# Kernel optimization log

Measured on AMD Instinct MI355X. Metric: run time of the kernel, lower is better.

Reference implementation:

```python
import jax, jax.numpy as jnp
import numpy as np

B, N, IN_F, OUT_F = 8, 2048, 256, 256
ALPHA = 0.2  # LeakyReLU negative slope
NEG_INF = -1e9


def setup_inputs() -> dict:
    key = jax.random.key(0)
    ks = jax.random.split(key, 8)
    h = jax.random.normal(ks[0], (B, N, IN_F), dtype=jnp.float32)
    adj = jax.random.randint(ks[1], (B, N, N), 0, 2, dtype=jnp.int32)
    # xavier-ish scaled params
    W_w = jax.random.normal(ks[2], (OUT_F, IN_F), dtype=jnp.float32) * (1.414 / np.sqrt(IN_F + OUT_F))
    W_b = jnp.zeros((OUT_F,), dtype=jnp.float32)
    ai_w = jax.random.normal(ks[3], (1, OUT_F), dtype=jnp.float32) * (1.414 / np.sqrt(OUT_F + 1))
    ai_b = jnp.zeros((1,), dtype=jnp.float32)
    aj_w = jax.random.normal(ks[4], (1, OUT_F), dtype=jnp.float32) * (1.414 / np.sqrt(OUT_F + 1))
    aj_b = jnp.zeros((1,), dtype=jnp.float32)
    return {"h": h, "adj": adj, "W_w": W_w, "W_b": W_b,
            "ai_w": ai_w, "ai_b": ai_b, "aj_w": aj_w, "aj_b": aj_b}


def reference(h, adj, W_w, W_b, ai_w, ai_b, aj_w, aj_b):
    # Wh: [B, N, F]
    Wh = jnp.einsum('bni,oi->bno', h, W_w) + W_b
    # additive attention scores (pos_embed_dim == 1 so the .view is a transpose)
    Wh1 = jnp.einsum('bnf,of->bno', Wh, ai_w) + ai_b        # [B, N, 1]
    Wh2 = jnp.einsum('bnf,of->bno', Wh, aj_w) + aj_b        # [B, N, 1]
    e = Wh1 + jnp.swapaxes(Wh2, 1, 2)                       # [B, N, N]
    e = jnp.where(e >= 0, e, ALPHA * e)                     # LeakyReLU
    attention = jnp.where(adj > 0, e, NEG_INF)
    attention = jax.nn.softmax(attention, axis=2)
    # dropout: inference mode (training=False) -> identity
    h_hat = jnp.einsum('bnm,bmf->bnf', attention, Wh)
    return jax.nn.elu(h_hat)  # concat=True
```

## Files before the change

### kernel.cpp

```cpp
#include <hip/hip_runtime.h>

typedef __bf16 bf16;
typedef _Float16 f16;
typedef __bf16 bf16x8 __attribute__((ext_vector_type(8)));
typedef _Float16 f16x8 __attribute__((ext_vector_type(8)));
typedef float  f32x4  __attribute__((ext_vector_type(4)));

#define B_  8
#define N_  2048
#define F_  256
#define NTOK (B_ * N_)
static constexpr float LOG2E = 1.44269504088896f;

__device__ __forceinline__ int detect_bf16(const void* h) {
    const unsigned* hw = (const unsigned*)h;
    unsigned w = hw[threadIdx.x & 63];
    unsigned ex = (w >> 7) & 0xFFu;
    unsigned long long b = __ballot(ex > 100u && ex < 150u);
    return __popcll(b) >= 40;
}

__device__ __forceinline__ float ldf(const void* p, int i, int isb) {
    return isb ? (float)((const bf16*)p)[i] : ((const float*)p)[i];
}

__device__ __forceinline__ bf16x8 cvt8(const float* p) {
    float4 a = *(const float4*)p;
    float4 b = *(const float4*)(p + 4);
    bf16x8 r;
    r[0]=(bf16)a.x; r[1]=(bf16)a.y; r[2]=(bf16)a.z; r[3]=(bf16)a.w;
    r[4]=(bf16)b.x; r[5]=(bf16)b.y; r[6]=(bf16)b.z; r[7]=(bf16)b.w;
    return r;
}

__device__ __forceinline__ size_t wht2_idx(int b, int f, int n) {
    int jc = n >> 6;
    int slot = ((n >> 3) & 7) ^ (f & 7);
    return (((size_t)(b * 32 + jc) * F_ + f) << 6) + (slot << 3) + (n & 7);
}

__global__ __launch_bounds__(256)
void k_wht(const void* __restrict__ hv, const void* __restrict__ Wv,
           const void* __restrict__ Wbv, const void* __restrict__ ai_wv,
           const void* __restrict__ ai_bv, const void* __restrict__ aj_wv,
           const void* __restrict__ aj_bv, bf16* __restrict__ WhT2,
           unsigned* __restrict__ adjw) {
    int isb = detect_bf16(hv);
    int ttile = blockIdx.x;
    int fg = threadIdx.x >> 6;
    int lane = threadIdx.x & 63;
    int T0 = ttile * 16;
    int m = lane & 15, quad = lane >> 4;

    f32x4 acc[4];
#pragma unroll
    for (int ft = 0; ft < 4; ++ft) acc[ft] = (f32x4){0.f, 0.f, 0.f, 0.f};

    if (isb) {
        const bf16* hp = (const bf16*)hv + (size_t)(T0 + m) * F_ + quad * 8;
        const bf16* wp = (const bf16*)Wv + (size_t)(fg * 64 + m) * F_ + quad * 8;
#pragma unroll
        for (int kk = 0; kk < F_; kk += 32) {
            bf16x8 hf = *(const bf16x8*)(hp + kk);
#pragma unroll
            for (int ft = 0; ft < 4; ++ft) {
                bf16x8 wf = *(const bf16x8*)(wp + (size_t)ft * 16 * F_ + kk);
                acc[ft] = __builtin_amdgcn_mfma_f32_16x16x32_bf16(wf, hf, acc[ft], 0, 0, 0);
            }
        }
    } else {
        const float* hp = (const float*)hv + (size_t)(T0 + m) * F_ + quad * 8;
        const float* wp = (const float*)Wv + (size_t)(fg * 64 + m) * F_ + quad * 8;
#pragma unroll
        for (int kk = 0; kk < F_; kk += 32) {
            bf16x8 hf = cvt8(hp + kk);
#pragma unroll
            for (int ft = 0; ft < 4; ++ft) {
                bf16x8 wf = cvt8(wp + (size_t)ft * 16 * F_ + kk);
                acc[ft] = __builtin_amdgcn_mfma_f32_16x16x32_bf16(wf, hf, acc[ft], 0, 0, 0);
            }
        }
    }
    int token = T0 + m;
    int b = token >> 11, n = token & (N_ - 1);
    float s_p = 0.f, t_p = 0.f;
#pragma unroll
    for (int ft = 0; ft < 4; ++ft)
#pragma unroll
        for (int r = 0; r < 4; ++r) {
            int f = fg * 64 + ft * 16 + quad * 4 + r;
            float v = acc[ft][r] + ldf(Wbv, f, isb);
            bf16 vb = (bf16)v;
            WhT2[wht2_idx(b, f, n)] = vb;
            float vr = (float)vb;
            s_p += vr * ldf(ai_wv, f, isb);
            t_p += vr * ldf(aj_wv, f, isb);
        }
    s_p += __shfl_down(s_p, 32, 64); s_p += __shfl_down(s_p, 16, 64);
    t_p += __shfl_down(t_p, 32, 64); t_p += __shfl_down(t_p, 16, 64);
    __shared__ float sred[4][16], tred[4][16];
    if (lane < 16) { sred[fg][lane] = s_p; tred[fg][lane] = t_p; }
    __syncthreads();
    if (threadIdx.x < 16) {
        int tid = threadIdx.x;
        int tok = T0 + tid;
        float ss = (sred[0][tid] + sred[1][tid] + sred[2][tid] + sred[3][tid]
                    + ldf(ai_bv, 0, isb)) * LOG2E;
        float tt = (tred[0][tid] + tred[1][tid] + tred[2][tid] + tred[3][tid]
                    + ldf(aj_bv, 0, isb)) * LOG2E;
        f16 th = (f16)tt, sh = (f16)ss;
        unsigned short tu, su;
        __builtin_memcpy(&tu, &th, 2);
        __builtin_memcpy(&su, &sh, 2);
        unsigned w0 = adjw[tok];
        adjw[tok] = (w0 & 0xFFFFu) | ((unsigned)tu << 16);
        unsigned w1 = adjw[NTOK + tok];
        adjw[NTOK + tok] = (w1 & 0xFFFFu) | ((unsigned)su << 16);
    }
}

__device__ __forceinline__ unsigned char pbits(uint4 a, uint4 b) {
    return (unsigned char)((a.x & 1u) | ((a.y & 1u) << 1) | ((a.z & 1u) << 2) |
                           ((a.w & 1u) << 3) | ((b.x & 1u) << 4) |
                           ((b.y & 1u) << 5) | ((b.z & 1u) << 6) |
                           ((b.w & 1u) << 7));
}

__device__ __forceinline__ void stageB(const bf16* tile, char* dst,
                                       int w, int lane) {
#pragma unroll
    for (int r = 0; r < 8; ++r) {
        int off = (w * 8 + r) * 1024;
        const bf16* g = tile + off / 2 + lane * 8;
        __builtin_amdgcn_global_load_lds(
            (const __attribute__((address_space(1))) unsigned*)g,
            (__attribute__((address_space(3))) unsigned*)(dst + off),
            16, 0, 0);
    }
}

__global__ __launch_bounds__(256)
void k_attn(const unsigned* __restrict__ adjw, const bf16* __restrict__ WhT2,
            const void* __restrict__ hv, void* __restrict__ outv) {
    int isb = detect_bf16(hv);
    int bid = blockIdx.x;
    int b = bid >> 6, itile = bid & 63, i0 = itile * 32;
    int tid = threadIdx.x;
    int w = tid >> 6, lane = tid & 63, m = lane & 15, q = lane >> 4;
    int mt = w >> 1, jh = w & 1;

    __shared__ __align__(16) char smem[70656];
    char* Bbuf0 = smem;
    char* Bbuf1 = smem + 32768;
    f16* tLDS   = (f16*)(smem + 65536);
    unsigned char* pack0 = (unsigned char*)(smem + 69632);
    unsigned char* pack1 = (unsigned char*)(smem + 69888);
    float* red  = (float*)smem;

    const bf16* batch_tiles = WhT2 + ((size_t)b * 32) * F_ * 64;

#pragma unroll
    for (int k = 0; k < 8; ++k) {
        int idx = k * 256 + tid;
        unsigned wv = adjw[b * N_ + idx];
        unsigned short us = (unsigned short)(wv >> 16);
        f16 tv; __builtin_memcpy(&tv, &us, 2);
        tLDS[idx] = tv;
    }
    int row = i0 + mt * 16 + m;
    unsigned swd = adjw[NTOK + b * N_ + row];
    unsigned short su = (unsigned short)(swd >> 16);
    f16 sh; __builtin_memcpy(&sh, &su, 2);
    float s2i = (float)sh;

    int prow = tid >> 3, ps = tid & 7;
    const unsigned* arow = adjw + ((size_t)(b * N_ + i0 + prow)) * N_ + ps * 8;
    {
        uint4 x0 = *(const uint4*)arow, x1 = *(const uint4*)(arow + 4);
        pack0[prow * 8 + ps] = pbits(x0, x1);
    }
    stageB(batch_tiles, Bbuf0, w, lane);
    __syncthreads();

    bf16x8 ones;
#pragma unroll
    for (int k = 0; k < 8; ++k) ones[k] = (bf16)1.0f;

    f32x4 acc[16];
#pragma unroll
    for (int ft = 0; ft < 16; ++ft) acc[ft] = (f32x4){0.f, 0.f, 0.f, 0.f};
    f32x4 acc_l = {0.f, 0.f, 0.f, 0.f};

    for (int c = 0; c < 32; ++c) {
        char* Bcur = (c & 1) ? Bbuf1 : Bbuf0;
        unsigned char* pcur = (c & 1) ? pack1 : pack0;
        uint4 aw0, aw1;
        bool pre = (c < 31);
        if (pre) {
            stageB(batch_tiles + (size_t)(c + 1) * F_ * 64,
                   (c & 1) ? Bbuf0 : Bbuf1, w, lane);
            aw0 = *(const uint4*)(arow + (size_t)(c + 1) * 64);
            aw1 = *(const uint4*)(arow + (size_t)(c + 1) * 64 + 4);
        }
        unsigned long long pb64 =
            *(const unsigned long long*)(pcur + (mt * 16 + m) * 8);
        unsigned bits8 = (unsigned)(pb64 >> ((jh * 4 + q) * 8)) & 0xFFu;
        f16x8 tv = *(const f16x8*)(tLDS + c * 64 + jh * 32 + q * 8);

        bf16x8 af;
#pragma unroll
        for (int qq = 0; qq < 8; ++qq) {
            float x = s2i + (float)tv[qq];
            x = fmaxf(x, 0.2f * x);
            float pv = ((bits8 >> qq) & 1u) ? __builtin_amdgcn_exp2f(x) : 0.f;
            af[qq] = (bf16)pv;
        }
        int sbase = (jh * 4 + q);
#pragma unroll
        for (int ft = 0; ft < 16; ++ft) {
            int fr = ft * 16 + m;
            int psl = sbase ^ (m & 7);
            bf16x8 bfr = *(const bf16x8*)(Bcur + fr * 128 + psl * 16);
            acc[ft] = __builtin_amdgcn_mfma_f32_16x16x32_bf16(af, bfr, acc[ft], 0, 0, 0);
        }
        acc_l = __builtin_amdgcn_mfma_f32_16x16x32_bf16(af, ones, acc_l, 0, 0, 0);
        if (pre)
            ((c & 1) ? pack0 : pack1)[prow * 8 + ps] = pbits(aw0, aw1);
        __syncthreads();
    }

    if (jh == 1) {
#pragma unroll
        for (int r = 0; r < 4; ++r) {
            int rr = mt * 16 + q * 4 + r;
#pragma unroll
            for (int ft = 0; ft < 16; ++ft)
                red[rr * 257 + ft * 16 + m] = acc[ft][r];
            if (m == 0) red[rr * 257 + 256] = acc_l[r];
        }
    }
    __syncthreads();
    if (jh == 0) {
#pragma unroll
        for (int r = 0; r < 4; ++r) {
            int rr = mt * 16 + q * 4 + r;
            float lf = acc_l[r] + red[rr * 257 + 256];
            float rl = (lf > 0.f) ? (1.f / lf) : 0.f;
            size_t ob = ((size_t)b * N_ + i0 + rr) * F_;
#pragma unroll
            for (int ft = 0; ft < 16; ++ft) {
                int f = ft * 16 + m;
                float v = acc[ft][r] + red[rr * 257 + f];
                v *= rl;
                v = (v > 0.f) ? v : (__builtin_amdgcn_exp2f(v * LOG2E) - 1.f);
                if (isb) ((bf16*)outv)[ob + f] = (bf16)v;
                else     ((float*)outv)[ob + f] = v;
            }
        }
    }
}

extern "C" void kernel_launch(void* const* d_in, const int* in_sizes, int n_in,
                              void* d_out, int out_size, void* d_ws, size_t ws_size,
                              hipStream_t stream) {
    (void)in_sizes; (void)n_in; (void)out_size; (void)ws_size;
    const void* h    = d_in[0];
    unsigned*   adjw = (unsigned*)d_in[1];
    const void* W_w  = d_in[2];
    const void* W_b  = d_in[3];
    const void* ai_w = d_in[4];
    const void* ai_b = d_in[5];
    const void* aj_w = d_in[6];
    const void* aj_b = d_in[7];

    bf16* WhT2 = (bf16*)d_ws;

    k_wht <<<dim3(1024), dim3(256), 0, stream>>>(h, W_w, W_b, ai_w, ai_b,
                                                 aj_w, aj_b, WhT2, adjw);
    k_attn<<<dim3(512),  dim3(256), 0, stream>>>(adjw, WhT2, h, d_out);
}
```

Baseline: 272.2 us.

## Load Wh tiles directly to registers, prepack full adjacency bitmask, split waves by feature half

The attention kernel stops staging Wh tiles through double-buffered LDS with global_load_lds. Each wave now reads its B fragments straight from global memory and covers both 16-row m-tiles for half of the feature columns, so each B fragment is reused across two MFMAs. The whole 32x2048 adjacency bitmask is packed into LDS once before the loop, and the per-iteration barrier becomes one barrier every four chunks. This saves LDS traffic and sync cost but depends on L2/L1 for B reuse across waves and blocks, and it adds a clamp on the exp2 argument.

```diff
diff --git a/kernel.cpp b/kernel.cpp
--- a/kernel.cpp
+++ b/kernel.cpp
@@ -119,26 +119,6 @@
     }
 }
 
-__device__ __forceinline__ unsigned char pbits(uint4 a, uint4 b) {
-    return (unsigned char)((a.x & 1u) | ((a.y & 1u) << 1) | ((a.z & 1u) << 2) |
-                           ((a.w & 1u) << 3) | ((b.x & 1u) << 4) |
-                           ((b.y & 1u) << 5) | ((b.z & 1u) << 6) |
-                           ((b.w & 1u) << 7));
-}
-
-__device__ __forceinline__ void stageB(const bf16* tile, char* dst,
-                                       int w, int lane) {
-#pragma unroll
-    for (int r = 0; r < 8; ++r) {
-        int off = (w * 8 + r) * 1024;
-        const bf16* g = tile + off / 2 + lane * 8;
-        __builtin_amdgcn_global_load_lds(
-            (const __attribute__((address_space(1))) unsigned*)g,
-            (__attribute__((address_space(3))) unsigned*)(dst + off),
-            16, 0, 0);
-    }
-}
-
 __global__ __launch_bounds__(256)
 void k_attn(const unsigned* __restrict__ adjw, const bf16* __restrict__ WhT2,
             const void* __restrict__ hv, void* __restrict__ outv) {
@@ -147,17 +127,13 @@
     int b = bid >> 6, itile = bid & 63, i0 = itile * 32;
     int tid = threadIdx.x;
     int w = tid >> 6, lane = tid & 63, m = lane & 15, q = lane >> 4;
-    int mt = w >> 1, jh = w & 1;
-
-    __shared__ __align__(16) char smem[70656];
-    char* Bbuf0 = smem;
-    char* Bbuf1 = smem + 32768;
-    f16* tLDS   = (f16*)(smem + 65536);
-    unsigned char* pack0 = (unsigned char*)(smem + 69632);
-    unsigned char* pack1 = (unsigned char*)(smem + 69888);
+    int jh = w & 1, fh = w >> 1;
+
+    __shared__ __align__(16) char smem[33280];
+    unsigned long long* pack64 = (unsigned long long*)smem;
+    f16*   tLDS = (f16*)(smem + 8448);
     float* red  = (float*)smem;
-
-    const bf16* batch_tiles = WhT2 + ((size_t)b * 32) * F_ * 64;
+    __shared__ float lLDS[2][32];
 
 #pragma unroll
     for (int k = 0; k < 8; ++k) {
@@ -167,94 +143,124 @@
         f16 tv; __builtin_memcpy(&tv, &us, 2);
         tLDS[idx] = tv;
     }
-    int row = i0 + mt * 16 + m;
-    unsigned swd = adjw[NTOK + b * N_ + row];
-    unsigned short su = (unsigned short)(swd >> 16);
-    f16 sh; __builtin_memcpy(&sh, &su, 2);
-    float s2i = (float)sh;
-
-    int prow = tid >> 3, ps = tid & 7;
-    const unsigned* arow = adjw + ((size_t)(b * N_ + i0 + prow)) * N_ + ps * 8;
+    float s2i0, s2i1;
     {
-        uint4 x0 = *(const uint4*)arow, x1 = *(const uint4*)(arow + 4);
-        pack0[prow * 8 + ps] = pbits(x0, x1);
-    }
-    stageB(batch_tiles, Bbuf0, w, lane);
+        unsigned sw0 = adjw[NTOK + b * N_ + i0 + m];
+        unsigned sw1 = adjw[NTOK + b * N_ + i0 + 16 + m];
+        unsigned short u0 = (unsigned short)(sw0 >> 16);
+        unsigned short u1 = (unsigned short)(sw1 >> 16);
+        f16 h0, h1;
+        __builtin_memcpy(&h0, &u0, 2); __builtin_memcpy(&h1, &u1, 2);
+        s2i0 = (float)h0; s2i1 = (float)h1;
+    }
+#pragma unroll
+    for (int k = 0; k < 4; ++k) {
+        int id = tid * 4 + k;
+        int prow = id >> 5, pc = id & 31;
+        const unsigned* src = adjw + ((size_t)(b * N_ + i0 + prow)) * N_ + pc * 64;
+        unsigned long long bits = 0;
+#pragma unroll
+        for (int w8 = 0; w8 < 16; ++w8) {
+            uint4 a = *(const uint4*)(src + w8 * 4);
+            bits |= (unsigned long long)((a.x & 1u) | ((a.y & 1u) << 1) |
+                                         ((a.z & 1u) << 2) | ((a.w & 1u) << 3))
+                    << (w8 * 4);
+        }
+        pack64[prow * 33 + pc] = bits;
+    }
     __syncthreads();
 
     bf16x8 ones;
 #pragma unroll
     for (int k = 0; k < 8; ++k) ones[k] = (bf16)1.0f;
 
-    f32x4 acc[16];
-#pragma unroll
-    for (int ft = 0; ft < 16; ++ft) acc[ft] = (f32x4){0.f, 0.f, 0.f, 0.f};
-    f32x4 acc_l = {0.f, 0.f, 0.f, 0.f};
+    f32x4 acc0[8], acc1[8];
+#pragma unroll
+    for (int ft = 0; ft < 8; ++ft) {
+        acc0[ft] = (f32x4){0.f, 0.f, 0.f, 0.f};
+        acc1[ft] = (f32x4){0.f, 0.f, 0.f, 0.f};
+    }
+    f32x4 acc_l0 = {0.f, 0.f, 0.f, 0.f}, acc_l1 = {0.f, 0.f, 0.f, 0.f};
+
+    int psl = (jh * 4 + q) ^ (m & 7);
+    const size_t tilestep = (size_t)F_ * 64;
+    const bf16* btile = WhT2 + (size_t)(b * 32) * tilestep +
+                        (size_t)(fh * 128) * 64 + m * 64 + psl * 8;
+    int byi = jh * 4 + q;
 
     for (int c = 0; c < 32; ++c) {
-        char* Bcur = (c & 1) ? Bbuf1 : Bbuf0;
-        unsigned char* pcur = (c & 1) ? pack1 : pack0;
-        uint4 aw0, aw1;
-        bool pre = (c < 31);
-        if (pre) {
-            stageB(batch_tiles + (size_t)(c + 1) * F_ * 64,
-                   (c & 1) ? Bbuf0 : Bbuf1, w, lane);
-            aw0 = *(const uint4*)(arow + (size_t)(c + 1) * 64);
-            aw1 = *(const uint4*)(arow + (size_t)(c + 1) * 64 + 4);
-        }
-        unsigned long long pb64 =
-            *(const unsigned long long*)(pcur + (mt * 16 + m) * 8);
-        unsigned bits8 = (unsigned)(pb64 >> ((jh * 4 + q) * 8)) & 0xFFu;
+        unsigned long long pb0 = pack64[m * 33 + c];
+        unsigned long long pb1 = pack64[(16 + m) * 33 + c];
+        unsigned bits0 = (unsigned)(pb0 >> (byi * 8)) & 0xFFu;
+        unsigned bits1 = (unsigned)(pb1 >> (byi * 8)) & 0xFFu;
         f16x8 tv = *(const f16x8*)(tLDS + c * 64 + jh * 32 + q * 8);
 
-        bf16x8 af;
+        bf16x8 af0, af1;
 #pragma unroll
         for (int qq = 0; qq < 8; ++qq) {
-            float x = s2i + (float)tv[qq];
-            x = fmaxf(x, 0.2f * x);
-            float pv = ((bits8 >> qq) & 1u) ? __builtin_amdgcn_exp2f(x) : 0.f;
-            af[qq] = (bf16)pv;
-        }
-        int sbase = (jh * 4 + q);
-#pragma unroll
-        for (int ft = 0; ft < 16; ++ft) {
-            int fr = ft * 16 + m;
-            int psl = sbase ^ (m & 7);
-            bf16x8 bfr = *(const bf16x8*)(Bcur + fr * 128 + psl * 16);
-            acc[ft] = __builtin_amdgcn_mfma_f32_16x16x32_bf16(af, bfr, acc[ft], 0, 0, 0);
-        }
-        acc_l = __builtin_amdgcn_mfma_f32_16x16x32_bf16(af, ones, acc_l, 0, 0, 0);
-        if (pre)
-            ((c & 1) ? pack0 : pack1)[prow * 8 + ps] = pbits(aw0, aw1);
-        __syncthreads();
-    }
-
+            float tvf = (float)tv[qq];
+            float x0 = s2i0 + tvf, x1 = s2i1 + tvf;
+            x0 = fmaxf(x0, 0.2f * x0);
+            x1 = fmaxf(x1, 0.2f * x1);
+            x0 = fminf(fmaxf(x0, -120.f), 60.f);
+            x1 = fminf(fmaxf(x1, -120.f), 60.f);
+            float p0 = ((bits0 >> qq) & 1u) ? __builtin_amdgcn_exp2f(x0) : 0.f;
+            float p1 = ((bits1 >> qq) & 1u) ? __builtin_amdgcn_exp2f(x1) : 0.f;
+            af0[qq] = (bf16)p0;
+            af1[qq] = (bf16)p1;
+        }
+        if (fh == 0) {
+            acc_l0 = __builtin_amdgcn_mfma_f32_16x16x32_bf16(af0, ones, acc_l0, 0, 0, 0);
+            acc_l1 = __builtin_amdgcn_mfma_f32_16x16x32_bf16(af1, ones, acc_l1, 0, 0, 0);
+        }
+        const bf16* bp = btile + (size_t)c * tilestep;
+#pragma unroll
+        for (int ft = 0; ft < 8; ++ft) {
+            bf16x8 bfr = *(const bf16x8*)(bp + ft * 1024);
+            acc0[ft] = __builtin_amdgcn_mfma_f32_16x16x32_bf16(af0, bfr, acc0[ft], 0, 0, 0);
+            acc1[ft] = __builtin_amdgcn_mfma_f32_16x16x32_bf16(af1, bfr, acc1[ft], 0, 0, 0);
+        }
+        if ((c & 3) == 3) __syncthreads();
+    }
+
+    __syncthreads();
+    if (fh == 0 && m == 0) {
+#pragma unroll
+        for (int r = 0; r < 4; ++r) {
+            lLDS[jh][q * 4 + r]      = acc_l0[r];
+            lLDS[jh][16 + q * 4 + r] = acc_l1[r];
+        }
+    }
     if (jh == 1) {
 #pragma unroll
         for (int r = 0; r < 4; ++r) {
-            int rr = mt * 16 + q * 4 + r;
-#pragma unroll
-            for (int ft = 0; ft < 16; ++ft)
-                red[rr * 257 + ft * 16 + m] = acc[ft][r];
-            if (m == 0) red[rr * 257 + 256] = acc_l[r];
+            int r0 = q * 4 + r, r1 = 16 + q * 4 + r;
+#pragma unroll
+            for (int ft = 0; ft < 8; ++ft) {
+                red[r0 * 260 + fh * 128 + ft * 16 + m] = acc0[ft][r];
+                red[r1 * 260 + fh * 128 + ft * 16 + m] = acc1[ft][r];
+            }
         }
     }
     __syncthreads();
     if (jh == 0) {
 #pragma unroll
-        for (int r = 0; r < 4; ++r) {
-            int rr = mt * 16 + q * 4 + r;
-            float lf = acc_l[r] + red[rr * 257 + 256];
-            float rl = (lf > 0.f) ? (1.f / lf) : 0.f;
-            size_t ob = ((size_t)b * N_ + i0 + rr) * F_;
-#pragma unroll
-            for (int ft = 0; ft < 16; ++ft) {
-                int f = ft * 16 + m;
-                float v = acc[ft][r] + red[rr * 257 + f];
-                v *= rl;
-                v = (v > 0.f) ? v : (__builtin_amdgcn_exp2f(v * LOG2E) - 1.f);
-                if (isb) ((bf16*)outv)[ob + f] = (bf16)v;
-                else     ((float*)outv)[ob + f] = v;
+        for (int mt = 0; mt < 2; ++mt) {
+#pragma unroll
+            for (int r = 0; r < 4; ++r) {
+                int row = mt * 16 + q * 4 + r;
+                float lf = lLDS[0][row] + lLDS[1][row];
+                float rl = (lf > 0.f) ? (1.f / lf) : 0.f;
+                size_t ob = ((size_t)b * N_ + i0 + row) * F_;
+#pragma unroll
+                for (int ft = 0; ft < 8; ++ft) {
+                    int f = fh * 128 + ft * 16 + m;
+                    float v = (mt ? acc1[ft][r] : acc0[ft][r]) + red[row * 260 + f];
+                    v *= rl;
+                    v = (v > 0.f) ? v : (__builtin_amdgcn_exp2f(v * LOG2E) - 1.f);
+                    if (isb) ((bf16*)outv)[ob + f] = (bf16)v;
+                    else     ((float*)outv)[ob + f] = v;
+                }
             }
         }
     }
```

Result: slower. 316.1 us (+16.1%).
